# Performance work log

Hardware: AMD Instinct MI355X
Metric: run time of the kernel (lower is better)

Reference implementation:

```python
import jax, jax.numpy as jnp
from jax import lax
import numpy as np

B, C_IN, C_OUT, H, W, K = 4, 128, 256, 64, 64, 3
KK = K * K
MID = C_IN // 4
EPS = 1e-5


def conv2d(x, w, b, pad, groups=1):
    out = lax.conv_general_dilated(x, w, (1, 1), [(pad, pad), (pad, pad)],
                                   feature_group_count=groups,
                                   dimension_numbers=('NCHW', 'OIHW', 'NCHW'))
    return out + b[None, :, None, None]


def bnorm(x, g, b, m, v):
    # inference-mode BatchNorm2d
    scale = (g / jnp.sqrt(v + EPS))
    return (x - m[None, :, None, None]) * scale[None, :, None, None] + b[None, :, None, None]


def bilinear_gather(x, py, px):
    # x: (B,C,H,W); py/px: (B,KK,H,W) float sample coords; zero outside bounds
    Bb, C, Hh, Ww = x.shape
    xf = x.reshape(Bb, C, Hh * Ww)
    y0 = jnp.floor(py)
    x0 = jnp.floor(px)
    wy1 = py - y0
    wx1 = px - x0

    def corner(yc, xc, wgt):
        valid = (yc >= 0) & (yc <= Hh - 1) & (xc >= 0) & (xc <= Ww - 1)
        yi = jnp.clip(yc, 0, Hh - 1).astype(jnp.int32)
        xi = jnp.clip(xc, 0, Ww - 1).astype(jnp.int32)
        idx = (yi * Ww + xi).reshape(Bb, -1)  # (B, KK*H*W)
        g = jax.vmap(lambda f, i: f[:, i])(xf, idx).reshape(Bb, C, *py.shape[1:])
        return g * (wgt * valid)[:, None]

    return (corner(y0, x0, (1 - wy1) * (1 - wx1))
            + corner(y0, x0 + 1, (1 - wy1) * wx1)
            + corner(y0 + 1, x0, wy1 * (1 - wx1))
            + corner(y0 + 1, x0 + 1, wy1 * wx1))


def deform_conv2d(x, offset, mask, w, b, pad=1):
    # modulated deformable conv v2, stride=1, dilation=1, groups=1, dg=1
    Bb, C, Hh, Ww = x.shape
    off = offset.reshape(Bb, KK, 2, Hh, Ww)  # (dy,dx) per kernel point
    k = jnp.arange(KK)
    ky = (k // K).astype(x.dtype)
    kx = (k % K).astype(x.dtype)
    py = (jnp.arange(Hh, dtype=x.dtype) - pad)[None, None, :, None] + ky[None, :, None, None] + off[:, :, 0]
    px = (jnp.arange(Ww, dtype=x.dtype) - pad)[None, None, None, :] + kx[None, :, None, None] + off[:, :, 1]
    val = bilinear_gather(x, py, px) * mask[:, None]  # (B,C,KK,H,W)
    return jnp.einsum('bckhw,ock->bohw', val, w.reshape(w.shape[0], C, KK)) + b[None, :, None, None]


def setup_inputs() -> dict:
    key = jax.random.key(0)
    ks = iter(jax.random.split(key, 40))

    def P(shape, scale=0.05):
        return jax.random.normal(next(ks), shape, jnp.float32) * scale

    d = {}
    d['x'] = jax.random.normal(next(ks), (B, C_IN, H, W), jnp.float32)
    # DCConv offset branch
    d['oc1_w'] = P((MID, C_IN, 3, 3)); d['oc1_b'] = P((MID,))
    d['obn_g'] = jnp.ones((MID,)); d['obn_b'] = jnp.zeros((MID,))
    d['obn_m'] = jnp.zeros((MID,)); d['obn_v'] = jnp.ones((MID,))
    d['oc2_w'] = P((2 * KK, MID, 3, 3), 0.01); d['oc2_b'] = P((2 * KK,), 0.01)
    # DCConv mask branch
    d['mc1_w'] = P((MID, C_IN, 3, 3)); d['mc1_b'] = P((MID,))
    d['mbn_g'] = jnp.ones((MID,)); d['mbn_b'] = jnp.zeros((MID,))
    d['mbn_m'] = jnp.zeros((MID,)); d['mbn_v'] = jnp.ones((MID,))
    d['mc2_w'] = P((KK, MID, 3, 3), 0.01); d['mc2_b'] = jnp.ones((KK,))
    # DCConv main weight
    d['dc_w'] = P((C_OUT, C_IN, 3, 3)); d['dc_b'] = jnp.zeros((C_OUT,))
    # contour branch: depthwise 3x3 + BN + ReLU + 1x1
    d['cb_dw_w'] = P((C_IN, 1, 3, 3)); d['cb_dw_b'] = P((C_IN,))
    d['cbn_g'] = jnp.ones((C_IN,)); d['cbn_b'] = jnp.zeros((C_IN,))
    d['cbn_m'] = jnp.zeros((C_IN,)); d['cbn_v'] = jnp.ones((C_IN,))
    d['cb_pw_w'] = P((C_OUT // 2, C_IN, 1, 1)); d['cb_pw_b'] = P((C_OUT // 2,))
    # spatial attention 7x7 -> 1 channel
    d['sa_w'] = P((1, C_OUT + C_OUT // 2, 7, 7)); d['sa_b'] = jnp.zeros((1,))
    # fusion 1x1 + BN + ReLU
    d['fu_w'] = P((C_OUT, C_OUT + C_OUT // 2, 1, 1)); d['fu_b'] = jnp.zeros((C_OUT,))
    d['fbn_g'] = jnp.ones((C_OUT,)); d['fbn_b'] = jnp.zeros((C_OUT,))
    d['fbn_m'] = jnp.zeros((C_OUT,)); d['fbn_v'] = jnp.ones((C_OUT,))
    return d


def reference(x, oc1_w, oc1_b, obn_g, obn_b, obn_m, obn_v, oc2_w, oc2_b,
              mc1_w, mc1_b, mbn_g, mbn_b, mbn_m, mbn_v, mc2_w, mc2_b,
              dc_w, dc_b, cb_dw_w, cb_dw_b, cbn_g, cbn_b, cbn_m, cbn_v,
              cb_pw_w, cb_pw_b, sa_w, sa_b, fu_w, fu_b, fbn_g, fbn_b, fbn_m, fbn_v):
    # DCConv: offsets + sigmoid masks + modulated deformable conv
    h = jax.nn.relu(bnorm(conv2d(x, oc1_w, oc1_b, 1), obn_g, obn_b, obn_m, obn_v))
    offset = conv2d(h, oc2_w, oc2_b, 1)
    hm = jax.nn.relu(bnorm(conv2d(x, mc1_w, mc1_b, 1), mbn_g, mbn_b, mbn_m, mbn_v))
    mask = jax.nn.sigmoid(conv2d(hm, mc2_w, mc2_b, 1))
    main_feat = deform_conv2d(x, offset, mask, dc_w, dc_b, pad=1)
    # contour branch
    hc = jax.nn.relu(bnorm(conv2d(x, cb_dw_w, cb_dw_b, 1, groups=C_IN), cbn_g, cbn_b, cbn_m, cbn_v))
    contour_feat = conv2d(hc, cb_pw_w, cb_pw_b, 0)
    combined = jnp.concatenate([main_feat, contour_feat], axis=1)
    attn = jax.nn.sigmoid(conv2d(combined, sa_w, sa_b, 3))
    combined = combined * attn
    return jax.nn.relu(bnorm(conv2d(combined, fu_w, fu_b, 0), fbn_g, fbn_b, fbn_m, fbn_v))
```

## Files before the change

kernel.cpp:

```cpp
#include <hip/hip_runtime.h>
#include <hip/hip_bf16.h>
#include <math.h>

#define BN   4
#define CIN  128
#define COUT 256
#define HWP  4096

typedef __hip_bfloat16 bf16;
typedef __attribute__((ext_vector_type(8))) short sh8;
typedef __attribute__((ext_vector_type(4))) float f32x4;

__device__ __forceinline__ float b2f(bf16 v) { return __bfloat162float(v); }
__device__ __forceinline__ float bflo(unsigned u) { return __uint_as_float(u << 16); }
__device__ __forceinline__ float bfhi(unsigned u) { return __uint_as_float(u & 0xffff0000u); }
__device__ __forceinline__ unsigned short f2bfbits(float f) {
    union { bf16 h; unsigned short u; } cv; cv.h = __float2bfloat16(f); return cv.u;
}
__device__ __forceinline__ float bfj(const uint4& c, int j) {
    unsigned u = (&c.x)[j >> 1];
    return (j & 1) ? bfhi(u) : bflo(u);
}

__global__ __launch_bounds__(256) void prep_all_kernel(
    const float* __restrict__ x, bf16* __restrict__ xt,
    const float* __restrict__ dc_w,
    const float* __restrict__ oc1_w, const float* __restrict__ oc1_b,
    const float* __restrict__ obn_g, const float* __restrict__ obn_b,
    const float* __restrict__ obn_m, const float* __restrict__ obn_v,
    const float* __restrict__ mc1_w, const float* __restrict__ mc1_b,
    const float* __restrict__ mbn_g, const float* __restrict__ mbn_b,
    const float* __restrict__ mbn_m, const float* __restrict__ mbn_v,
    const float* __restrict__ fu_w, const float* __restrict__ fu_b,
    const float* __restrict__ fbn_g, const float* __restrict__ fbn_b,
    const float* __restrict__ fbn_m, const float* __restrict__ fbn_v,
    const float* __restrict__ sa_w,
    const float* __restrict__ oc2_w, const float* __restrict__ mc2_w,
    const float* __restrict__ cb_pw_w,
    const float* __restrict__ cb_dw_b, const float* __restrict__ cbn_g,
    const float* __restrict__ cbn_b, const float* __restrict__ cbn_m,
    const float* __restrict__ cbn_v,
    bf16* __restrict__ wBf2, bf16* __restrict__ wCf2, float* __restrict__ ab,
    bf16* __restrict__ wFf, bf16* __restrict__ wSAf, float* __restrict__ fab,
    bf16* __restrict__ wDf, bf16* __restrict__ wPf, float* __restrict__ dwab)
{
    __shared__ bf16 t[64][136];
    if (blockIdx.x < 256) {
        const int b = blockIdx.x >> 6, chunk = blockIdx.x & 63;
        const int pos0 = chunk * 64;
        const int tid = threadIdx.x;
        const int lane = tid & 63, wv = tid >> 6;
        const float* xb = x + (size_t)b * CIN * HWP + pos0 + lane;
        #pragma unroll 4
        for (int j = 0; j < 32; j++) {
            int ci = wv * 32 + j;
            t[lane][ci] = __float2bfloat16(xb[(size_t)ci * HWP]);
        }
        __syncthreads();
        const int p = tid >> 2, cig = tid & 3;
        uint4* dst = (uint4*)(xt + ((size_t)b * HWP + pos0 + p) * 128 + cig * 32);
        const uint4* src = (const uint4*)&t[p][cig * 32];
        #pragma unroll
        for (int q = 0; q < 4; q++) dst[q] = src[q];
        return;
    }

    int o = (blockIdx.x - 256) * 256 + threadIdx.x;
    if (o < 294912) {
        int j = o & 7, o2 = o >> 3;
        int lane = o2 & 63, t_ = o2 >> 6;
        int l16 = lane & 15, quad = lane >> 4;
        int mt = t_ & 3, t2 = t_ >> 2;
        int kt = t2 % 18, t3 = t2 / 18;
        int h = t3 & 1, wv = t3 >> 1;
        int co = wv * 64 + mt * 16 + l16;
        int kkh = kt * 32 + quad * 8 + j;
        int k = kkh >> 6, ci = h * 64 + (kkh & 63);
        wBf2[o] = __float2bfloat16(dc_w[co * 1152 + ci * 9 + k]);
    } else if (o < 368640) {
        int idx = o - 294912;
        int j = idx & 7, o2 = idx >> 3;
        int lane = o2 & 63, t_ = o2 >> 6;
        int l16 = lane & 15, quad = lane >> 4;
        int kt = t_ % 18, t2 = t_ / 18;
        int h = t2 & 1, wv = t2 >> 1;
        int co = wv * 16 + l16;
        int kkh = kt * 32 + quad * 8 + j;
        int k = kkh >> 6, ci = h * 64 + (kkh & 63);
        float v = (co < 32) ? oc1_w[co * 1152 + ci * 9 + k]
                            : mc1_w[(co - 32) * 1152 + ci * 9 + k];
        wCf2[idx] = __float2bfloat16(v);
    } else if (o < 368704) {
        int c = o - 368640;
        float g, bb, m, vv, bias;
        if (c < 32) { g = obn_g[c]; bb = obn_b[c]; m = obn_m[c]; vv = obn_v[c]; bias = oc1_b[c]; }
        else { int c2 = c - 32; g = mbn_g[c2]; bb = mbn_b[c2]; m = mbn_m[c2]; vv = mbn_v[c2]; bias = mc1_b[c2]; }
        float alpha = g / sqrtf(vv + 1e-5f);
        ab[c] = alpha;
        ab[64 + c] = (bias - m) * alpha + bb;
    } else if (o < 467008) {
        int idx = o - 368704;
        int j = idx & 7, o2 = idx >> 3;
        int lane = o2 & 63, t_ = o2 >> 6;
        int l16 = lane & 15, quad = lane >> 4;
        int mt = t_ & 3, t2 = t_ >> 2;
        int kt = t2 % 12, wv = t2 / 12;
        int co = wv * 64 + mt * 16 + l16;
        int kk = kt * 32 + quad * 8 + j;
        wFf[idx] = __float2bfloat16(fu_w[co * 384 + kk]);
    } else if (o < 491584) {
        int idx = o - 467008;
        int j = idx & 7, o2 = idx >> 3;
        int lane = o2 & 63, t_ = o2 >> 6;
        int l16 = lane & 15, quad = lane >> 4;
        int kt = t_ % 12, wv = t_ / 12;
        int jr = wv * 16 + l16;
        int kk = kt * 32 + quad * 8 + j;
        wSAf[idx] = (jr < 49) ? __float2bfloat16(sa_w[kk * 49 + jr]) : __float2bfloat16(0.f);
    } else if (o < 491840) {
        int co = o - 491584;
        float alpha = fbn_g[co] / sqrtf(fbn_v[co] + 1e-5f);
        fab[co] = alpha;
        fab[256 + co] = (fu_b[co] - fbn_m[co]) * alpha + fbn_b[co];
    } else if (o < 510272) {
        int idx = o - 491840;
        int j = idx & 7, o2 = idx >> 3;
        int lane = o2 & 63, t_ = o2 >> 6;
        int l16 = lane & 15, quad = lane >> 4;
        int mt = t_ & 1, kt = t_ >> 1;
        int co = mt * 16 + l16;
        int kk = kt * 32 + quad * 8 + j;
        int k = kk >> 6, c = kk & 63;
        float v = 0.f;
        if (co < 18 && c < 32) v = oc2_w[co * 288 + c * 9 + k];
        else if (co >= 18 && co < 27 && c >= 32) v = mc2_w[(co - 18) * 288 + (c - 32) * 9 + k];
        wDf[idx] = __float2bfloat16(v);
    } else if (o < 526656) {
        int idx = o - 510272;
        int j = idx & 7, o2 = idx >> 3;
        int lane = o2 & 63, t_ = o2 >> 6;
        int l16 = lane & 15, quad = lane >> 4;
        int wv = t_ >> 3, kt = (t_ >> 1) & 3, mt = t_ & 1;
        int co = wv * 32 + mt * 16 + l16;
        int kk = kt * 32 + quad * 8 + j;
        wPf[idx] = __float2bfloat16(cb_pw_w[co * 128 + kk]);
    } else if (o < 526784) {
        int c = o - 526656;
        float alpha = cbn_g[c] / sqrtf(cbn_v[c] + 1e-5f);
        dwab[c] = alpha;
        dwab[128 + c] = (cb_dw_b[c] - cbn_m[c]) * alpha + cbn_b[c];
    }
}

__global__ __launch_bounds__(256) void conv1_mfma_kernel(
    const bf16* __restrict__ xt, const bf16* __restrict__ wCf2, const float* __restrict__ ab,
    bf16* __restrict__ ht)
{
    __shared__ __align__(16) bf16 val[32][584];

    const int bid = blockIdx.x;
    const int b = (bid & 7) >> 1;
    const int tile = ((bid >> 3) << 1) | (bid & 1);
    const int pos0 = tile * 32;
    const int y = tile >> 1, x0 = (tile & 1) * 32;
    const int tid = threadIdx.x;
    const int lane = tid & 63, wv = tid >> 6;
    const int quad = lane >> 4, l16 = lane & 15;

    f32x4 acc[2] = {f32x4{0,0,0,0}, f32x4{0,0,0,0}};
    const bf16* xtb = xt + (size_t)b * HWP * 128;

    #pragma unroll
    for (int h = 0; h < 2; h++) {
        if (h) __syncthreads();
        {
            const int cig = tid & 7, pix = tid >> 3;
            const int ci0 = h * 64 + cig * 8;
            const int xxp = x0 + pix;
            #pragma unroll
            for (int k = 0; k < 9; k++) {
                int yy = y + k / 3 - 1, xx = xxp + k % 3 - 1;
                bool valid = (yy >= 0 && yy <= 63 && xx >= 0 && xx <= 63);
                uint4 c = {0, 0, 0, 0};
                if (valid) c = *(const uint4*)(xtb + (size_t)(yy * 64 + xx) * 128 + ci0);
                *(uint4*)&val[pix][k * 64 + cig * 8] = c;
            }
        }
        __syncthreads();

        const bf16* wl0 = wCf2 + ((size_t)(wv * 2 + h) * 18) * 512 + lane * 8;
        const bf16* vb0 = &val[l16][quad * 8];
        const bf16* vb1 = &val[16 + l16][quad * 8];
        for (int kt = 0; kt < 18; kt++) {
            sh8 af = *(const sh8*)(wl0 + kt * 512);
            sh8 b0 = *(const sh8*)(vb0 + kt * 32);
            sh8 b1 = *(const sh8*)(vb1 + kt * 32);
            acc[0] = __builtin_amdgcn_mfma_f32_16x16x32_bf16(af, b0, acc[0], 0, 0, 0);
            acc[1] = __builtin_amdgcn_mfma_f32_16x16x32_bf16(af, b1, acc[1], 0, 0, 0);
        }
    }

    const int co0 = wv * 16 + quad * 4;
    #pragma unroll
    for (int ph = 0; ph < 2; ph++) {
        float o0 = fmaxf(acc[ph][0] * ab[co0 + 0] + ab[64 + co0 + 0], 0.f);
        float o1 = fmaxf(acc[ph][1] * ab[co0 + 1] + ab[64 + co0 + 1], 0.f);
        float o2 = fmaxf(acc[ph][2] * ab[co0 + 2] + ab[64 + co0 + 2], 0.f);
        float o3 = fmaxf(acc[ph][3] * ab[co0 + 3] + ab[64 + co0 + 3], 0.f);
        uint2 pk;
        pk.x = (unsigned)f2bfbits(o0) | ((unsigned)f2bfbits(o1) << 16);
        pk.y = (unsigned)f2bfbits(o2) | ((unsigned)f2bfbits(o3) << 16);
        *(uint2*)(ht + ((size_t)b * HWP + pos0 + ph * 16 + l16) * 64 + co0) = pk;
    }
}

__global__ __launch_bounds__(256) void dwpw_kernel(
    const bf16* __restrict__ xt, const float* __restrict__ dw_w, const float* __restrict__ dwab,
    const bf16* __restrict__ wPf, const float* __restrict__ pw_b, bf16* __restrict__ combined)
{
    __shared__ float wl[1152];
    __shared__ float abl[256];
    __shared__ __align__(16) bf16 vdw[16][136];
    const int bid = blockIdx.x;
    const int b = bid >> 8, tile = bid & 255;
    const int pos0 = tile * 16;
    const int y = tile >> 2, x0 = (tile & 3) * 16;
    const int tid = threadIdx.x;
    for (int i = tid; i < 1152; i += 256) wl[i] = dw_w[i];
    abl[tid] = dwab[tid];
    __syncthreads();

    {
        const int cig = tid & 15, pix = tid >> 4;
        const int ci0 = cig * 8;
        const int xxp = x0 + pix;
        const bf16* xtb = xt + (size_t)b * HWP * 128;
        float g[8] = {0, 0, 0, 0, 0, 0, 0, 0};
        #pragma unroll
        for (int k = 0; k < 9; k++) {
            int yy = y + k / 3 - 1, xx = xxp + k % 3 - 1;
            if (yy < 0 || yy > 63 || xx < 0 || xx > 63) continue;
            uint4 c = *(const uint4*)(xtb + (size_t)(yy * 64 + xx) * 128 + ci0);
            #pragma unroll
            for (int j = 0; j < 8; j++)
                g[j] += wl[(ci0 + j) * 9 + k] * bfj(c, j);
        }
        uint4 pk;
        float o[8];
        #pragma unroll
        for (int j = 0; j < 8; j++)
            o[j] = fmaxf(g[j] * abl[ci0 + j] + abl[128 + ci0 + j], 0.f);
        pk.x = (unsigned)f2bfbits(o[0]) | ((unsigned)f2bfbits(o[1]) << 16);
        pk.y = (unsigned)f2bfbits(o[2]) | ((unsigned)f2bfbits(o[3]) << 16);
        pk.z = (unsigned)f2bfbits(o[4]) | ((unsigned)f2bfbits(o[5]) << 16);
        pk.w = (unsigned)f2bfbits(o[6]) | ((unsigned)f2bfbits(o[7]) << 16);
        *(uint4*)&vdw[pix][ci0] = pk;
    }
    __syncthreads();

    const int lane = tid & 63, wv = tid >> 6;
    const int quad = lane >> 4, l16 = lane & 15;
    f32x4 acc[2] = {f32x4{0,0,0,0}, f32x4{0,0,0,0}};
    const bf16* fb = &vdw[l16][quad * 8];
    const bf16* wl0 = wPf + (size_t)wv * 4096 + lane * 8;
    #pragma unroll
    for (int kt = 0; kt < 4; kt++) {
        sh8 bf = *(const sh8*)(fb + kt * 32);
        #pragma unroll
        for (int mt = 0; mt < 2; mt++) {
            sh8 af = *(const sh8*)(wl0 + (kt * 2 + mt) * 512);
            acc[mt] = __builtin_amdgcn_mfma_f32_16x16x32_bf16(af, bf, acc[mt], 0, 0, 0);
        }
    }

    bf16* ct = combined + ((size_t)b * HWP + pos0 + l16) * 384 + 256;
    #pragma unroll
    for (int mt = 0; mt < 2; mt++) {
        int co_b = wv * 32 + mt * 16 + quad * 4;
        uint2 pk;
        pk.x = (unsigned)f2bfbits(acc[mt][0] + pw_b[co_b])     | ((unsigned)f2bfbits(acc[mt][1] + pw_b[co_b + 1]) << 16);
        pk.y = (unsigned)f2bfbits(acc[mt][2] + pw_b[co_b + 2]) | ((unsigned)f2bfbits(acc[mt][3] + pw_b[co_b + 3]) << 16);
        *(uint2*)(ct + co_b) = pk;
    }
}

__global__ __launch_bounds__(256) void deform_kernel(
    const bf16* __restrict__ xt, const bf16* __restrict__ ht, const bf16* __restrict__ wDf,
    const float* __restrict__ oc2_b, const float* __restrict__ mc2_b,
    const bf16* __restrict__ wBf2, const float* __restrict__ bias, bf16* __restrict__ combined)
{
    __shared__ __align__(16) bf16 val[32][584];
    __shared__ int   ti[288][4];
    __shared__ float tw[288][4];
    __shared__ float loff[18][32];
    __shared__ float lmsk[9][32];

    const int bid = blockIdx.x;
    const int b = (bid & 7) >> 1;
    const int tile = ((bid >> 3) << 1) | (bid & 1);
    const int pos0 = tile * 32;
    const int y = tile >> 1, x0 = (tile & 1) * 32;
    const int tid = threadIdx.x;
    const int lane = tid & 63, wv = tid >> 6;
    const int quad = lane >> 4, l16 = lane & 15;

    {
        const int cig = tid & 7, pix = tid >> 3;
        const int xxp = x0 + pix;
        const bf16* hb = ht + (size_t)b * HWP * 64;
        #pragma unroll
        for (int k = 0; k < 9; k++) {
            int yy = y + k / 3 - 1, xx = xxp + k % 3 - 1;
            bool valid = (yy >= 0 && yy <= 63 && xx >= 0 && xx <= 63);
            uint4 c = {0, 0, 0, 0};
            if (valid) c = *(const uint4*)(hb + (size_t)(yy * 64 + xx) * 64 + cig * 8);
            *(uint4*)&val[pix][k * 64 + cig * 8] = c;
        }
    }
    __syncthreads();
    {
        const int ph = wv >> 1, mt = wv & 1;
        f32x4 acc2 = {0, 0, 0, 0};
        const bf16* wl0 = wDf + ((size_t)mt * 64 + lane) * 8;
        const bf16* vbase = &val[ph * 16 + l16][quad * 8];
        for (int kt = 0; kt < 18; kt++) {
            sh8 af = *(const sh8*)(wl0 + kt * 1024);
            sh8 bf = *(const sh8*)(vbase + kt * 32);
            acc2 = __builtin_amdgcn_mfma_f32_16x16x32_bf16(af, bf, acc2, 0, 0, 0);
        }
        const int pix2 = ph * 16 + l16;
        #pragma unroll
        for (int r = 0; r < 4; r++) {
            int co = mt * 16 + quad * 4 + r;
            if (co < 18) {
                loff[co][pix2] = acc2[r] + oc2_b[co];
            } else if (co < 27) {
                float s = acc2[r] + mc2_b[co - 18];
                lmsk[co - 18][pix2] = 1.f / (1.f + expf(-s));
            }
        }
    }
    __syncthreads();

    for (int e = tid; e < 288; e += 256) {
        int k = e >> 5, pix = e & 31;
        int pos = pos0 + pix;
        int yp = pos >> 6, xc = pos & 63;
        float offy = loff[2 * k][pix];
        float offx = loff[2 * k + 1][pix];
        float m = lmsk[k][pix];
        float py = (float)(yp - 1 + k / 3) + offy;
        float px = (float)(xc - 1 + k % 3) + offx;
        float fy = floorf(py), fx = floorf(px);
        float wy1 = py - fy, wx1 = px - fx;
        int y0 = (int)fy, x0c = (int)fx;
        int y1 = y0 + 1, x1 = x0c + 1;
        bool vy0 = (y0 >= 0 && y0 <= 63), vy1 = (y1 >= 0 && y1 <= 63);
        bool vx0 = (x0c >= 0 && x0c <= 63), vx1 = (x1 >= 0 && x1 <= 63);
        int cy0 = min(max(y0, 0), 63), cy1 = min(max(y1, 0), 63);
        int cx0 = min(max(x0c, 0), 63), cx1 = min(max(x1, 0), 63);
        ti[e][0] = cy0 * 64 + cx0;  tw[e][0] = (vy0 && vx0) ? (1.f - wy1) * (1.f - wx1) * m : 0.f;
        ti[e][1] = cy0 * 64 + cx1;  tw[e][1] = (vy0 && vx1) ? (1.f - wy1) * wx1 * m : 0.f;
        ti[e][2] = cy1 * 64 + cx0;  tw[e][2] = (vy1 && vx0) ? wy1 * (1.f - wx1) * m : 0.f;
        ti[e][3] = cy1 * 64 + cx1;  tw[e][3] = (vy1 && vx1) ? wy1 * wx1 * m : 0.f;
    }
    __syncthreads();

    f32x4 acc[4][2] = {{f32x4{0,0,0,0}, f32x4{0,0,0,0}}, {f32x4{0,0,0,0}, f32x4{0,0,0,0}},
                       {f32x4{0,0,0,0}, f32x4{0,0,0,0}}, {f32x4{0,0,0,0}, f32x4{0,0,0,0}}};
    const bf16* xtb = xt + (size_t)b * HWP * 128;

    #pragma unroll
    for (int h = 0; h < 2; h++) {
        if (h) __syncthreads();
        {
            const int cig = tid & 7, pix = tid >> 3;
            const int ci0 = h * 64 + cig * 8;
            for (int k = 0; k < 9; k++) {
                const int e = k * 32 + pix;
                const int i0 = ti[e][0], i1 = ti[e][1], i2 = ti[e][2], i3 = ti[e][3];
                const float w0 = tw[e][0], w1 = tw[e][1], w2 = tw[e][2], w3 = tw[e][3];
                uint4 c0 = *(const uint4*)(xtb + (size_t)i0 * 128 + ci0);
                uint4 c1 = *(const uint4*)(xtb + (size_t)i1 * 128 + ci0);
                uint4 c2 = *(const uint4*)(xtb + (size_t)i2 * 128 + ci0);
                uint4 c3 = *(const uint4*)(xtb + (size_t)i3 * 128 + ci0);
                float g[8];
                #pragma unroll
                for (int j = 0; j < 8; j++)
                    g[j] = w0 * bfj(c0, j) + w1 * bfj(c1, j) + w2 * bfj(c2, j) + w3 * bfj(c3, j);
                uint4 pk;
                pk.x = (unsigned)f2bfbits(g[0]) | ((unsigned)f2bfbits(g[1]) << 16);
                pk.y = (unsigned)f2bfbits(g[2]) | ((unsigned)f2bfbits(g[3]) << 16);
                pk.z = (unsigned)f2bfbits(g[4]) | ((unsigned)f2bfbits(g[5]) << 16);
                pk.w = (unsigned)f2bfbits(g[6]) | ((unsigned)f2bfbits(g[7]) << 16);
                *(uint4*)&val[pix][k * 64 + cig * 8] = pk;
            }
        }
        __syncthreads();

        const bf16* wl0 = wBf2 + ((size_t)(wv * 2 + h) * 72) * 512 + lane * 8;
        const bf16* vb0 = &val[l16][quad * 8];
        const bf16* vb1 = &val[16 + l16][quad * 8];
        sh8 af[4], afn[4];
        #pragma unroll
        for (int mt = 0; mt < 4; mt++) af[mt] = *(const sh8*)(wl0 + mt * 512);
        for (int kt = 0; kt < 18; kt++) {
            sh8 b0 = *(const sh8*)(vb0 + kt * 32);
            sh8 b1 = *(const sh8*)(vb1 + kt * 32);
            if (kt < 17) {
                #pragma unroll
                for (int mt = 0; mt < 4; mt++)
                    afn[mt] = *(const sh8*)(wl0 + ((kt + 1) * 4 + mt) * 512);
            }
            #pragma unroll
            for (int mt = 0; mt < 4; mt++) {
                acc[mt][0] = __builtin_amdgcn_mfma_f32_16x16x32_bf16(af[mt], b0, acc[mt][0], 0, 0, 0);
                acc[mt][1] = __builtin_amdgcn_mfma_f32_16x16x32_bf16(af[mt], b1, acc[mt][1], 0, 0, 0);
            }
            #pragma unroll
            for (int mt = 0; mt < 4; mt++) af[mt] = afn[mt];
        }
    }

    #pragma unroll
    for (int ph = 0; ph < 2; ph++) {
        bf16* ct = combined + ((size_t)b * HWP + pos0 + ph * 16 + l16) * 384;
        #pragma unroll
        for (int mt = 0; mt < 4; mt++) {
            int co_b = wv * 64 + mt * 16 + quad * 4;
            uint2 pk;
            pk.x = (unsigned)f2bfbits(acc[mt][ph][0] + bias[co_b])     | ((unsigned)f2bfbits(acc[mt][ph][1] + bias[co_b + 1]) << 16);
            pk.y = (unsigned)f2bfbits(acc[mt][ph][2] + bias[co_b + 2]) | ((unsigned)f2bfbits(acc[mt][ph][3] + bias[co_b + 3]) << 16);
            *(uint2*)(ct + co_b) = pk;
        }
    }
}

__global__ __launch_bounds__(256) void sa_gemm_kernel(
    const bf16* __restrict__ combined, const bf16* __restrict__ wSAf, float* __restrict__ part)
{
    const int bid = blockIdx.x;
    const int b = bid >> 8, tile = bid & 255;
    const int pos0 = tile * 16;
    const int tid = threadIdx.x;
    const int lane = tid & 63, wv = tid >> 6;
    const int quad = lane >> 4, l16 = lane & 15;

    f32x4 acc = {0, 0, 0, 0};
    const bf16* fb = combined + ((size_t)b * HWP + pos0 + l16) * 384 + quad * 8;
    const bf16* wl0 = wSAf + (size_t)wv * 6144 + lane * 8;

    sh8 af = *(const sh8*)(wl0);
    sh8 bf = *(const sh8*)(fb);
    sh8 afn, bfn;
    for (int kt = 0; kt < 12; kt++) {
        if (kt < 11) {
            afn = *(const sh8*)(wl0 + (kt + 1) * 512);
            bfn = *(const sh8*)(fb + (kt + 1) * 32);
        }
        acc = __builtin_amdgcn_mfma_f32_16x16x32_bf16(af, bf, acc, 0, 0, 0);
        af = afn; bf = bfn;
    }
    #pragma unroll
    for (int r = 0; r < 4; r++) {
        int j = wv * 16 + quad * 4 + r;
        if (j < 49) part[(size_t)(j * BN + b) * HWP + pos0 + l16] = acc[r];
    }
}

__global__ __launch_bounds__(256) void fuse_kernel(
    const bf16* __restrict__ combined, const float* __restrict__ part, const float* __restrict__ sa_b,
    const bf16* __restrict__ wFf, const float* __restrict__ fab, float* __restrict__ out)
{
    __shared__ float sattn[16][17];
    __shared__ float lattn[16];

    const int bid = blockIdx.x;
    const int b = bid >> 8, tile = bid & 255;
    const int pos0 = tile * 16;
    const int y = tile >> 2, x0 = (tile & 3) * 16;
    const int tid = threadIdx.x;

    {
        const int px = tid & 15, g = tid >> 4;
        const int xp = x0 + px;
        float s = 0.f;
        for (int j = g; j < 49; j += 16) {
            int yy = y + j / 7 - 3, xx = xp + j % 7 - 3;
            if (yy < 0 || yy > 63 || xx < 0 || xx > 63) continue;
            s += part[(size_t)(j * BN + b) * HWP + yy * 64 + xx];
        }
        sattn[px][g] = s;
    }
    __syncthreads();
    if (tid < 16) {
        float t = sa_b[0];
        #pragma unroll
        for (int g = 0; g < 16; g++) t += sattn[tid][g];
        lattn[tid] = 1.f / (1.f + expf(-t));
    }
    __syncthreads();

    const int lane = tid & 63, wv = tid >> 6;
    const int quad = lane >> 4, l16 = lane & 15;

    f32x4 acc[4] = {f32x4{0,0,0,0}, f32x4{0,0,0,0}, f32x4{0,0,0,0}, f32x4{0,0,0,0}};
    const bf16* fb = combined + ((size_t)b * HWP + pos0 + l16) * 384 + quad * 8;
    const bf16* wl0 = wFf + (size_t)wv * 24576 + lane * 8;

    sh8 af[4], afn[4], bf, bfn;
    bf = *(const sh8*)(fb);
    #pragma unroll
    for (int mt = 0; mt < 4; mt++) af[mt] = *(const sh8*)(wl0 + mt * 512);
    for (int kt = 0; kt < 12; kt++) {
        if (kt < 11) {
            bfn = *(const sh8*)(fb + (kt + 1) * 32);
            #pragma unroll
            for (int mt = 0; mt < 4; mt++)
                afn[mt] = *(const sh8*)(wl0 + ((kt + 1) * 4 + mt) * 512);
        }
        #pragma unroll
        for (int mt = 0; mt < 4; mt++)
            acc[mt] = __builtin_amdgcn_mfma_f32_16x16x32_bf16(af[mt], bf, acc[mt], 0, 0, 0);
        bf = bfn;
        #pragma unroll
        for (int mt = 0; mt < 4; mt++) af[mt] = afn[mt];
    }

    float a = lattn[l16];
    float* op = out + (size_t)b * COUT * HWP + pos0 + l16;
    #pragma unroll
    for (int mt = 0; mt < 4; mt++) {
        int co_b = wv * 64 + mt * 16 + quad * 4;
        #pragma unroll
        for (int r = 0; r < 4; r++) {
            int co = co_b + r;
            float o = fmaxf(acc[mt][r] * a * fab[co] + fab[256 + co], 0.f);
            op[(size_t)co * HWP] = o;
        }
    }
}

extern "C" void kernel_launch(void* const* d_in, const int* in_sizes, int n_in,
                              void* d_out, int out_size, void* d_ws, size_t ws_size,
                              hipStream_t stream)
{
    const float* x      = (const float*)d_in[0];
    const float* oc1_w  = (const float*)d_in[1];
    const float* oc1_b  = (const float*)d_in[2];
    const float* obn_g  = (const float*)d_in[3];
    const float* obn_b  = (const float*)d_in[4];
    const float* obn_m  = (const float*)d_in[5];
    const float* obn_v  = (const float*)d_in[6];
    const float* oc2_w  = (const float*)d_in[7];
    const float* oc2_b  = (const float*)d_in[8];
    const float* mc1_w  = (const float*)d_in[9];
    const float* mc1_b  = (const float*)d_in[10];
    const float* mbn_g  = (const float*)d_in[11];
    const float* mbn_b  = (const float*)d_in[12];
    const float* mbn_m  = (const float*)d_in[13];
    const float* mbn_v  = (const float*)d_in[14];
    const float* mc2_w  = (const float*)d_in[15];
    const float* mc2_b  = (const float*)d_in[16];
    const float* dc_w   = (const float*)d_in[17];
    const float* dc_b   = (const float*)d_in[18];
    const float* cb_dw_w= (const float*)d_in[19];
    const float* cb_dw_b= (const float*)d_in[20];
    const float* cbn_g  = (const float*)d_in[21];
    const float* cbn_b  = (const float*)d_in[22];
    const float* cbn_m  = (const float*)d_in[23];
    const float* cbn_v  = (const float*)d_in[24];
    const float* cb_pw_w= (const float*)d_in[25];
    const float* cb_pw_b= (const float*)d_in[26];
    const float* sa_w   = (const float*)d_in[27];
    const float* sa_b   = (const float*)d_in[28];
    const float* fu_w   = (const float*)d_in[29];
    const float* fu_b   = (const float*)d_in[30];
    const float* fbn_g  = (const float*)d_in[31];
    const float* fbn_b  = (const float*)d_in[32];
    const float* fbn_m  = (const float*)d_in[33];
    const float* fbn_v  = (const float*)d_in[34];

    bf16*  ht    = (bf16*)d_ws;
    bf16*  comb  = ht + 1048576;
    float* part  = (float*)(comb + 6291456);
    bf16*  xt    = (bf16*)(part + 802816);
    bf16*  wBf2  = xt + 2097152;
    bf16*  wCf2  = wBf2 + 294912;
    float* ab    = (float*)(wCf2 + 73728);
    bf16*  wFf   = (bf16*)(ab + 128);
    bf16*  wSAf  = wFf + 98304;
    float* fab   = (float*)(wSAf + 24576);
    bf16*  wDf   = (bf16*)(fab + 512);
    bf16*  wPf   = wDf + 18432;
    float* dwab  = (float*)(wPf + 16384);

    float* out = (float*)d_out;

    prep_all_kernel<<<256 + 2058, 256, 0, stream>>>(
        x, xt,
        dc_w, oc1_w, oc1_b, obn_g, obn_b, obn_m, obn_v,
        mc1_w, mc1_b, mbn_g, mbn_b, mbn_m, mbn_v,
        fu_w, fu_b, fbn_g, fbn_b, fbn_m, fbn_v, sa_w,
        oc2_w, mc2_w, cb_pw_w, cb_dw_b, cbn_g, cbn_b, cbn_m, cbn_v,
        wBf2, wCf2, ab, wFf, wSAf, fab, wDf, wPf, dwab);
    conv1_mfma_kernel<<<512, 256, 0, stream>>>(xt, wCf2, ab, ht);
    dwpw_kernel<<<1024, 256, 0, stream>>>(xt, cb_dw_w, dwab, wPf, cb_pw_b, comb);
    deform_kernel<<<512, 256, 0, stream>>>(xt, ht, wDf, oc2_b, mc2_b, wBf2, dc_b, comb);
    sa_gemm_kernel<<<1024, 256, 0, stream>>>(comb, wSAf, part);
    fuse_kernel<<<1024, 256, 0, stream>>>(comb, part, sa_b, wFf, fab, out);
}
```

Before: 207.0 us.

## Fuse spatial-attention channel GEMM into deform and dwpw epilogues

Removes the separate sa_gemm kernel by computing each producer's partial spatial-attention projection from its own output tile. The tile is staged in shared memory and multiplied by the matching slice of wSAf: channels 0-255 in deform_kernel and 256-383 in dwpw_kernel. The two partial sums go to separate buffers, which fuse_kernel adds. This saves one launch and a full re-read of the combined tensor, at the cost of extra shared-memory passes and syncs in both producers and a second partial buffer read in fuse.

```diff
diff --git a/kernel.cpp b/kernel.cpp
--- a/kernel.cpp
+++ b/kernel.cpp
@@ -216,7 +216,8 @@
 
 __global__ __launch_bounds__(256) void dwpw_kernel(
     const bf16* __restrict__ xt, const float* __restrict__ dw_w, const float* __restrict__ dwab,
-    const bf16* __restrict__ wPf, const float* __restrict__ pw_b, bf16* __restrict__ combined)
+    const bf16* __restrict__ wPf, const float* __restrict__ pw_b,
+    const bf16* __restrict__ wSAf, bf16* __restrict__ combined, float* __restrict__ part_b)
 {
     __shared__ float wl[1152];
     __shared__ float abl[256];
@@ -282,12 +283,39 @@
         pk.y = (unsigned)f2bfbits(acc[mt][2] + pw_b[co_b + 2]) | ((unsigned)f2bfbits(acc[mt][3] + pw_b[co_b + 3]) << 16);
         *(uint2*)(ct + co_b) = pk;
     }
+
+    __syncthreads();
+    bf16* ct2 = &vdw[0][0];
+    #pragma unroll
+    for (int mt = 0; mt < 2; mt++) {
+        int co_b = wv * 32 + mt * 16 + quad * 4;
+        uint2 pk;
+        pk.x = (unsigned)f2bfbits(acc[mt][0] + pw_b[co_b])     | ((unsigned)f2bfbits(acc[mt][1] + pw_b[co_b + 1]) << 16);
+        pk.y = (unsigned)f2bfbits(acc[mt][2] + pw_b[co_b + 2]) | ((unsigned)f2bfbits(acc[mt][3] + pw_b[co_b + 3]) << 16);
+        *(uint2*)(ct2 + l16 * 136 + co_b) = pk;
+    }
+    __syncthreads();
+
+    f32x4 sacc = {0, 0, 0, 0};
+    const bf16* awl = wSAf + (size_t)wv * 6144 + lane * 8;
+    #pragma unroll
+    for (int kt2 = 0; kt2 < 4; kt2++) {
+        sh8 af = *(const sh8*)(awl + (8 + kt2) * 512);
+        sh8 bf2 = *(const sh8*)(ct2 + l16 * 136 + kt2 * 32 + quad * 8);
+        sacc = __builtin_amdgcn_mfma_f32_16x16x32_bf16(af, bf2, sacc, 0, 0, 0);
+    }
+    #pragma unroll
+    for (int r = 0; r < 4; r++) {
+        int j = wv * 16 + quad * 4 + r;
+        if (j < 49) part_b[(size_t)(j * BN + b) * HWP + pos0 + l16] = sacc[r];
+    }
 }
 
 __global__ __launch_bounds__(256) void deform_kernel(
     const bf16* __restrict__ xt, const bf16* __restrict__ ht, const bf16* __restrict__ wDf,
     const float* __restrict__ oc2_b, const float* __restrict__ mc2_b,
-    const bf16* __restrict__ wBf2, const float* __restrict__ bias, bf16* __restrict__ combined)
+    const bf16* __restrict__ wBf2, const float* __restrict__ bias,
+    const bf16* __restrict__ wSAf, bf16* __restrict__ combined, float* __restrict__ part_a)
 {
     __shared__ __align__(16) bf16 val[32][584];
     __shared__ int   ti[288][4];
@@ -422,6 +450,7 @@
         }
     }
 
+    uint2 pko[4][2];
     #pragma unroll
     for (int ph = 0; ph < 2; ph++) {
         bf16* ct = combined + ((size_t)b * HWP + pos0 + ph * 16 + l16) * 384;
@@ -432,44 +461,45 @@
             pk.x = (unsigned)f2bfbits(acc[mt][ph][0] + bias[co_b])     | ((unsigned)f2bfbits(acc[mt][ph][1] + bias[co_b + 1]) << 16);
             pk.y = (unsigned)f2bfbits(acc[mt][ph][2] + bias[co_b + 2]) | ((unsigned)f2bfbits(acc[mt][ph][3] + bias[co_b + 3]) << 16);
             *(uint2*)(ct + co_b) = pk;
-        }
-    }
-}
-
-__global__ __launch_bounds__(256) void sa_gemm_kernel(
-    const bf16* __restrict__ combined, const bf16* __restrict__ wSAf, float* __restrict__ part)
-{
-    const int bid = blockIdx.x;
-    const int b = bid >> 8, tile = bid & 255;
-    const int pos0 = tile * 16;
-    const int tid = threadIdx.x;
-    const int lane = tid & 63, wv = tid >> 6;
-    const int quad = lane >> 4, l16 = lane & 15;
-
-    f32x4 acc = {0, 0, 0, 0};
-    const bf16* fb = combined + ((size_t)b * HWP + pos0 + l16) * 384 + quad * 8;
-    const bf16* wl0 = wSAf + (size_t)wv * 6144 + lane * 8;
-
-    sh8 af = *(const sh8*)(wl0);
-    sh8 bf = *(const sh8*)(fb);
-    sh8 afn, bfn;
-    for (int kt = 0; kt < 12; kt++) {
-        if (kt < 11) {
-            afn = *(const sh8*)(wl0 + (kt + 1) * 512);
-            bfn = *(const sh8*)(fb + (kt + 1) * 32);
-        }
-        acc = __builtin_amdgcn_mfma_f32_16x16x32_bf16(af, bf, acc, 0, 0, 0);
-        af = afn; bf = bfn;
-    }
-    #pragma unroll
-    for (int r = 0; r < 4; r++) {
-        int j = wv * 16 + quad * 4 + r;
-        if (j < 49) part[(size_t)(j * BN + b) * HWP + pos0 + l16] = acc[r];
+            pko[mt][ph] = pk;
+        }
+    }
+
+    __syncthreads();
+    bf16* ctile = &val[0][0];
+    #pragma unroll
+    for (int ph = 0; ph < 2; ph++) {
+        int pix = ph * 16 + l16;
+        #pragma unroll
+        for (int mt = 0; mt < 4; mt++) {
+            int co_b = wv * 64 + mt * 16 + quad * 4;
+            *(uint2*)(ctile + pix * 264 + co_b) = pko[mt][ph];
+        }
+    }
+    __syncthreads();
+
+    f32x4 sacc[2] = {f32x4{0,0,0,0}, f32x4{0,0,0,0}};
+    const bf16* awl = wSAf + (size_t)wv * 6144 + lane * 8;
+    for (int kt = 0; kt < 8; kt++) {
+        sh8 af = *(const sh8*)(awl + kt * 512);
+        sh8 b0 = *(const sh8*)(ctile + l16 * 264 + kt * 32 + quad * 8);
+        sh8 b1 = *(const sh8*)(ctile + (16 + l16) * 264 + kt * 32 + quad * 8);
+        sacc[0] = __builtin_amdgcn_mfma_f32_16x16x32_bf16(af, b0, sacc[0], 0, 0, 0);
+        sacc[1] = __builtin_amdgcn_mfma_f32_16x16x32_bf16(af, b1, sacc[1], 0, 0, 0);
+    }
+    #pragma unroll
+    for (int ph = 0; ph < 2; ph++) {
+        #pragma unroll
+        for (int r = 0; r < 4; r++) {
+            int j = wv * 16 + quad * 4 + r;
+            if (j < 49) part_a[(size_t)(j * BN + b) * HWP + pos0 + ph * 16 + l16] = sacc[ph][r];
+        }
     }
 }
 
 __global__ __launch_bounds__(256) void fuse_kernel(
-    const bf16* __restrict__ combined, const float* __restrict__ part, const float* __restrict__ sa_b,
+    const bf16* __restrict__ combined, const float* __restrict__ part_a, const float* __restrict__ part_b,
+    const float* __restrict__ sa_b,
     const bf16* __restrict__ wFf, const float* __restrict__ fab, float* __restrict__ out)
 {
     __shared__ float sattn[16][17];
@@ -488,7 +518,8 @@
         for (int j = g; j < 49; j += 16) {
             int yy = y + j / 7 - 3, xx = xp + j % 7 - 3;
             if (yy < 0 || yy > 63 || xx < 0 || xx > 63) continue;
-            s += part[(size_t)(j * BN + b) * HWP + yy * 64 + xx];
+            size_t idx = (size_t)(j * BN + b) * HWP + yy * 64 + xx;
+            s += part_a[idx] + part_b[idx];
         }
         sattn[px][g] = s;
     }
@@ -581,19 +612,20 @@
     const float* fbn_m  = (const float*)d_in[33];
     const float* fbn_v  = (const float*)d_in[34];
 
-    bf16*  ht    = (bf16*)d_ws;
-    bf16*  comb  = ht + 1048576;
-    float* part  = (float*)(comb + 6291456);
-    bf16*  xt    = (bf16*)(part + 802816);
-    bf16*  wBf2  = xt + 2097152;
-    bf16*  wCf2  = wBf2 + 294912;
-    float* ab    = (float*)(wCf2 + 73728);
-    bf16*  wFf   = (bf16*)(ab + 128);
-    bf16*  wSAf  = wFf + 98304;
-    float* fab   = (float*)(wSAf + 24576);
-    bf16*  wDf   = (bf16*)(fab + 512);
-    bf16*  wPf   = wDf + 18432;
-    float* dwab  = (float*)(wPf + 16384);
+    bf16*  ht     = (bf16*)d_ws;
+    bf16*  comb   = ht + 1048576;
+    float* part_a = (float*)(comb + 6291456);
+    float* part_b = part_a + 802816;
+    bf16*  xt     = (bf16*)(part_b + 802816);
+    bf16*  wBf2   = xt + 2097152;
+    bf16*  wCf2   = wBf2 + 294912;
+    float* ab     = (float*)(wCf2 + 73728);
+    bf16*  wFf    = (bf16*)(ab + 128);
+    bf16*  wSAf   = wFf + 98304;
+    float* fab    = (float*)(wSAf + 24576);
+    bf16*  wDf    = (bf16*)(fab + 512);
+    bf16*  wPf    = wDf + 18432;
+    float* dwab   = (float*)(wPf + 16384);
 
     float* out = (float*)d_out;
 
@@ -605,8 +637,7 @@
         oc2_w, mc2_w, cb_pw_w, cb_dw_b, cbn_g, cbn_b, cbn_m, cbn_v,
         wBf2, wCf2, ab, wFf, wSAf, fab, wDf, wPf, dwab);
     conv1_mfma_kernel<<<512, 256, 0, stream>>>(xt, wCf2, ab, ht);
-    dwpw_kernel<<<1024, 256, 0, stream>>>(xt, cb_dw_w, dwab, wPf, cb_pw_b, comb);
-    deform_kernel<<<512, 256, 0, stream>>>(xt, ht, wDf, oc2_b, mc2_b, wBf2, dc_b, comb);
-    sa_gemm_kernel<<<1024, 256, 0, stream>>>(comb, wSAf, part);
-    fuse_kernel<<<1024, 256, 0, stream>>>(comb, part, sa_b, wFf, fab, out);
-}
+    dwpw_kernel<<<1024, 256, 0, stream>>>(xt, cb_dw_w, dwab, wPf, cb_pw_b, wSAf, comb, part_b);
+    deform_kernel<<<512, 256, 0, stream>>>(xt, ht, wDf, oc2_b, mc2_b, wBf2, dc_b, wSAf, comb, part_a);
+    fuse_kernel<<<1024, 256, 0, stream>>>(comb, part_a, part_b, sa_b, wFf, fab, out);
+}
```

Measured after the change: 200.1 us. 1.03x faster.
